# Performance work log

Measured on AMD Instinct MI355X. Metric: run time of the kernel, lower is better.

Reference implementation:

```python
import jax, jax.numpy as jnp
import numpy as np
from jax import lax

DN = ('NCHW', 'OIHW', 'NCHW')

def conv3x3(x, w):
    return lax.conv_general_dilated(x, w, (1, 1), 'SAME', dimension_numbers=DN)

def conv1x1(x, w, b):
    # w: [O, C], x: [B, C, H, W]
    return jnp.einsum('oc,bchw->bohw', w, x) + b[None, :, None, None]

def bn_relu(x, p):
    # p: [2, C] -> (scale, shift), eval-mode folded BatchNorm + ReLU
    return jax.nn.relu(x * p[0][None, :, None, None] + p[1][None, :, None, None])

def pam(y, Wb, bb, Wc, bc, Wd, bd, alpha):
    B, C, H, W = y.shape
    n = H * W
    b_ = conv1x1(y, Wb, bb).reshape(B, -1, n)   # [B, C/8, N]
    c_ = conv1x1(y, Wc, bc).reshape(B, -1, n)   # [B, C/8, N]
    d_ = conv1x1(y, Wd, bd).reshape(B, C, n)    # [B, C, N]
    energy = jnp.einsum('bkn,bkm->bnm', b_, c_)  # [B, N, N]
    attn = jax.nn.softmax(energy, axis=-1)
    feat = jnp.einsum('bcm,bnm->bcn', d_, attn).reshape(B, C, H, W)
    return alpha[0] * feat + y

def cam(y, beta):
    B, C, H, W = y.shape
    xf = y.reshape(B, C, H * W)
    energy = jnp.einsum('bcn,bdn->bcd', xf, xf)  # [B, C, C]
    energy = jnp.max(energy, axis=-1, keepdims=True) - energy
    attn = jax.nn.softmax(energy, axis=-1)
    feat = jnp.einsum('bcd,bdn->bcn', attn, xf).reshape(B, C, H, W)
    return beta[0] * feat + y

def reference(x, Wp1, bnp1, Wc1, bnc1, Wb, bb, Wc, bc, Wd, bd, alpha, beta,
              Wp2, bnp2, Wc2, bnc2, Wout, bout, Wp3, bp3, Wc3, bc3):
    feat_p = bn_relu(conv3x3(x, Wp1), bnp1)
    feat_p = pam(feat_p, Wb, bb, Wc, bc, Wd, bd, alpha)
    feat_p = bn_relu(conv3x3(feat_p, Wp2), bnp2)

    feat_c = bn_relu(conv3x3(x, Wc1), bnc1)
    feat_c = cam(feat_c, beta)
    feat_c = bn_relu(conv3x3(feat_c, Wc2), bnc2)

    fusion = feat_p + feat_c
    out_main = jax.nn.sigmoid(conv1x1(fusion, Wout, bout))
    out_p = jax.nn.sigmoid(conv1x1(feat_p, Wp3, bp3))
    out_c = jax.nn.sigmoid(conv1x1(feat_c, Wc3, bc3))
    return (out_main, out_p, out_c)

def setup_inputs() -> dict:
    key = jax.random.key(0)
    ks = jax.random.split(key, 24)
    Cin, Ci, Ck, NC = 512, 128, 16, 19
    B, H, W = 8, 64, 64
    s = lambda k, shape, scale=0.05: jax.random.normal(k, shape, jnp.float32) * scale
    return {
        'x': jax.random.normal(ks[0], (B, Cin, H, W), jnp.float32),
        'Wp1': s(ks[1], (Ci, Cin, 3, 3)), 'bnp1': jnp.stack([jnp.ones(Ci), jnp.zeros(Ci)]),
        'Wc1': s(ks[2], (Ci, Cin, 3, 3)), 'bnc1': jnp.stack([jnp.ones(Ci), jnp.zeros(Ci)]),
        'Wb': s(ks[3], (Ck, Ci)), 'bb': s(ks[4], (Ck,)),
        'Wc': s(ks[5], (Ck, Ci)), 'bc': s(ks[6], (Ck,)),
        'Wd': s(ks[7], (Ci, Ci)), 'bd': s(ks[8], (Ci,)),
        'alpha': jax.random.normal(ks[9], (1,), jnp.float32) * 0.5,
        'beta': jax.random.normal(ks[10], (1,), jnp.float32) * 0.5,
        'Wp2': s(ks[11], (Ci, Ci, 3, 3)), 'bnp2': jnp.stack([jnp.ones(Ci), jnp.zeros(Ci)]),
        'Wc2': s(ks[12], (Ci, Ci, 3, 3)), 'bnc2': jnp.stack([jnp.ones(Ci), jnp.zeros(Ci)]),
        'Wout': s(ks[13], (NC, Ci)), 'bout': s(ks[14], (NC,)),
        'Wp3': s(ks[15], (NC, Ci)), 'bp3': s(ks[16], (NC,)),
        'Wc3': s(ks[17], (NC, Ci)), 'bc3': s(ks[18], (NC,)),
    }
```

## Files before the change

kernel.cpp:

```cpp
#include <hip/hip_runtime.h>
#include <math.h>


typedef __attribute__((ext_vector_type(8)))  short short8;
typedef __attribute__((ext_vector_type(16))) float f32x16;

__device__ inline unsigned short f2bf(float f) {
    union { float f; unsigned u; } v; v.f = f;
    unsigned r = v.u + 0x7fffu + ((v.u >> 16) & 1u);
    return (unsigned short)(r >> 16);
}
__device__ inline float bf2f(unsigned short h) {
    union { unsigned u; float f; } v; v.u = ((unsigned)h) << 16;
    return v.f;
}

__global__ __launch_bounds__(256) void wpack_kernel(
    const float* __restrict__ W, unsigned short* __restrict__ wp, int Cin, int total)
{
    int idx = blockIdx.x * 256 + threadIdx.x;
    if (idx >= total) return;
    int chunk = idx / 18432;
    int rem   = idx - chunk * 18432;
    int tap   = rem >> 11;
    int rem2  = rem & 2047;
    int g     = rem2 >> 10;
    int co    = (rem2 >> 3) & 127;
    int ci8   = rem2 & 7;
    int cin   = (chunk << 4) + (g << 3) + ci8;
    wp[idx] = f2bf(W[((size_t)co * Cin + cin) * 9 + tap]);
}

__global__ __launch_bounds__(256) void wpack_split_kernel(
    const float* __restrict__ W, unsigned short* __restrict__ wph,
    unsigned short* __restrict__ wpl, int Cin, int total)
{
    int idx = blockIdx.x * 256 + threadIdx.x;
    if (idx >= total) return;
    int chunk = idx / 18432;
    int rem   = idx - chunk * 18432;
    int tap   = rem >> 11;
    int rem2  = rem & 2047;
    int g     = rem2 >> 10;
    int co    = (rem2 >> 3) & 127;
    int ci8   = rem2 & 7;
    int cin   = (chunk << 4) + (g << 3) + ci8;
    float w = W[((size_t)co * Cin + cin) * 9 + tap];
    unsigned short hi = f2bf(w);
    wph[idx] = hi;
    wpl[idx] = f2bf(w - bf2f(hi));
}

__global__ __launch_bounds__(256, 4) void conv3x3_merged(
    const float* __restrict__ xin,
    const unsigned short* __restrict__ wpp,
    const unsigned short* __restrict__ wph, const unsigned short* __restrict__ wpl,
    const float* __restrict__ bnp, const float* __restrict__ bnc,
    float* __restrict__ outP, float* __restrict__ outC,
    unsigned short* __restrict__ outh, unsigned short* __restrict__ outl)
{
    const int t   = threadIdx.x;
    const int w2  = t >> 6;
    const int xh  = w2 & 1;
    const int wy  = w2 >> 1;
    const int ln  = t & 63;
    const int l31 = ln & 31;
    const int g   = ln >> 5;
    const int y   = blockIdx.x;
    const int co0 = blockIdx.y << 6;
    const int b   = blockIdx.z;

    const int sr   = t >> 6;
    const int sx   = t & 63;
    const int sgy  = y - 1 + sr;
    const bool sv  = (t < 192) && ((unsigned)sgy < 64u);
    const int spid = sr * 66 + sx + 1;

    __shared__ __align__(16) unsigned short Xh[2][3168];
    __shared__ __align__(16) unsigned short Xo[2][3168];

    for (int i = t; i < 792; i += 256) {
        uint4 z; z.x = 0; z.y = 0; z.z = 0; z.w = 0;
        ((uint4*)Xh)[i] = z;
        ((uint4*)Xo)[i] = z;
    }

    const int co = co0 + (wy << 5) + l31;
    const unsigned short* wPb = wpp + (size_t)(g << 10) + ((size_t)co << 3);
    const unsigned short* wHb = wph + (size_t)(g << 10) + ((size_t)co << 3);
    const unsigned short* wLb = wpl + (size_t)(g << 10) + ((size_t)co << 3);
    const float* xsrc = xin + ((size_t)b << 21) + (sgy << 6) + sx;

    const f32x16 zero = {0,0,0,0,0,0,0,0,0,0,0,0,0,0,0,0};
    f32x16 ap = zero, ac = zero;

    float xv[16];
    if (sv) {
#pragma unroll
        for (int c = 0; c < 16; c++) xv[c] = xsrc[(size_t)c << 12];
    }
    __syncthreads();

    if (sv) {
        unsigned short th[16], tl[16];
#pragma unroll
        for (int c = 0; c < 16; c++) {
            unsigned short hi = f2bf(xv[c]);
            th[c] = hi; tl[c] = f2bf(xv[c] - bf2f(hi));
        }
        *(uint4*)&Xh[0][spid << 3]          = ((uint4*)th)[0];
        *(uint4*)&Xh[0][1584 + (spid << 3)] = ((uint4*)th)[1];
        *(uint4*)&Xo[0][spid << 3]          = ((uint4*)tl)[0];
        *(uint4*)&Xo[0][1584 + (spid << 3)] = ((uint4*)tl)[1];
    }

    int cur = 0;
    for (int ch = 0; ch < 32; ++ch) {
        __syncthreads();
        const bool pf = (ch < 31);
        if (pf && sv) {
#pragma unroll
            for (int c = 0; c < 16; c++)
                xv[c] = xsrc[((size_t)(ch + 1) << 16) + ((size_t)c << 12)];
        }
        const size_t wo = (size_t)ch * 18432;
#pragma unroll 3
        for (int tap = 0; tap < 9; ++tap) {
            const int dy = tap / 3, dx = tap - dy * 3;
            const int xi = (g ? 1584 : 0) + (((dy * 66) + (xh << 5) + l31 + dx) << 3);
            short8 vap = *(const short8*)(wPb + wo + tap * 2048);
            short8 vah = *(const short8*)(wHb + wo + tap * 2048);
            short8 val = *(const short8*)(wLb + wo + tap * 2048);
            short8 bh_ = *(const short8*)&Xh[cur][xi];
            short8 bl_ = *(const short8*)&Xo[cur][xi];
            ap = __builtin_amdgcn_mfma_f32_32x32x16_bf16(vap, bh_, ap, 0, 0, 0);
            ac = __builtin_amdgcn_mfma_f32_32x32x16_bf16(vah, bh_, ac, 0, 0, 0);
            ac = __builtin_amdgcn_mfma_f32_32x32x16_bf16(vah, bl_, ac, 0, 0, 0);
            ac = __builtin_amdgcn_mfma_f32_32x32x16_bf16(val, bh_, ac, 0, 0, 0);
        }
        if (pf && sv) {
            unsigned short th[16], tl[16];
#pragma unroll
            for (int c = 0; c < 16; c++) {
                unsigned short hi = f2bf(xv[c]);
                th[c] = hi; tl[c] = f2bf(xv[c] - bf2f(hi));
            }
            const int nb = cur ^ 1;
            *(uint4*)&Xh[nb][spid << 3]          = ((uint4*)th)[0];
            *(uint4*)&Xh[nb][1584 + (spid << 3)] = ((uint4*)th)[1];
            *(uint4*)&Xo[nb][spid << 3]          = ((uint4*)tl)[0];
            *(uint4*)&Xo[nb][1584 + (spid << 3)] = ((uint4*)tl)[1];
        }
        cur ^= 1;
    }

    const int x = (xh << 5) + l31;
#pragma unroll
    for (int r = 0; r < 16; r++) {
        int c2 = co0 + (wy << 5) + (r & 3) + ((r >> 2) << 3) + (g << 2);
        size_t o = (((size_t)b * 128 + c2) << 12) + (y << 6) + x;
        float vp = fmaf(ap[r], bnp[c2], bnp[128 + c2]);
        vp = vp > 0.f ? vp : 0.f;
        outP[o] = vp;
        float vc = fmaf(ac[r], bnc[c2], bnc[128 + c2]);
        vc = vc > 0.f ? vc : 0.f;
        outC[o] = vc;
        unsigned short hi = f2bf(vc);
        outh[o] = hi;
        outl[o] = f2bf(vc - bf2f(hi));
    }
}

__global__ __launch_bounds__(256, 4) void conv3x3_bf(
    const unsigned short* __restrict__ xin, int Cin,
    const unsigned short* __restrict__ wpk, const float* __restrict__ bn,
    float* __restrict__ out_f32)
{
    const int t   = threadIdx.x;
    const int w2  = t >> 6;
    const int xh  = w2 & 1;
    const int wy  = w2 >> 1;
    const int ln  = t & 63;
    const int l31 = ln & 31;
    const int g   = ln >> 5;
    const int y   = blockIdx.x;
    const int co0 = blockIdx.y << 6;
    const int b   = blockIdx.z;

    const int sr   = t >> 6;
    const int sx   = t & 63;
    const int sgy  = y - 1 + sr;
    const bool sv  = (t < 192) && ((unsigned)sgy < 64u);
    const int spid = sr * 66 + sx + 1;

    __shared__ __align__(16) unsigned short Xl[2][3168];

    for (int i = t; i < 792; i += 256) {
        uint4 z; z.x = 0; z.y = 0; z.z = 0; z.w = 0;
        ((uint4*)Xl)[i] = z;
    }

    const int co = co0 + (wy << 5) + l31;
    const unsigned short* wB = wpk + (size_t)(g << 10) + ((size_t)co << 3);
    const unsigned short* xsrc = xin + (((size_t)b * Cin) << 12) + (sgy << 6) + sx;

    const f32x16 zero = {0,0,0,0,0,0,0,0,0,0,0,0,0,0,0,0};
    f32x16 acc = zero;

    unsigned short xv[16];
    if (sv) {
#pragma unroll
        for (int c = 0; c < 16; c++) xv[c] = xsrc[(size_t)c << 12];
    }
    __syncthreads();

    if (sv) {
        *(uint4*)&Xl[0][spid << 3]          = ((uint4*)xv)[0];
        *(uint4*)&Xl[0][1584 + (spid << 3)] = ((uint4*)xv)[1];
    }

    const int nchunks = Cin >> 4;
    int cur = 0;
    for (int ch = 0; ch < nchunks; ++ch) {
        __syncthreads();
        const bool pf = (ch < nchunks - 1);
        if (pf && sv) {
#pragma unroll
            for (int c = 0; c < 16; c++)
                xv[c] = xsrc[((size_t)(ch + 1) << 16) + ((size_t)c << 12)];
        }
        const size_t wo = (size_t)ch * 18432;
#pragma unroll 3
        for (int tap = 0; tap < 9; ++tap) {
            const int dy = tap / 3, dx = tap - dy * 3;
            const int xi = (g ? 1584 : 0) + (((dy * 66) + (xh << 5) + l31 + dx) << 3);
            short8 a  = *(const short8*)(wB + wo + tap * 2048);
            short8 b0 = *(const short8*)&Xl[cur][xi];
            acc = __builtin_amdgcn_mfma_f32_32x32x16_bf16(a, b0, acc, 0, 0, 0);
        }
        if (pf && sv) {
            const int nb = cur ^ 1;
            *(uint4*)&Xl[nb][spid << 3]          = ((uint4*)xv)[0];
            *(uint4*)&Xl[nb][1584 + (spid << 3)] = ((uint4*)xv)[1];
        }
        cur ^= 1;
    }

    const int x = (xh << 5) + l31;
#pragma unroll
    for (int r = 0; r < 16; r++) {
        int c2 = co0 + (wy << 5) + (r & 3) + ((r >> 2) << 3) + (g << 2);
        float v = fmaf(acc[r], bn[c2], bn[128 + c2]);
        v = v > 0.f ? v : 0.f;
        out_f32[(((size_t)b * 128 + c2) << 12) + (y << 6) + x] = v;
    }
}

__global__ __launch_bounds__(256, 4) void conv3x3_hilo_bf(
    const unsigned short* __restrict__ xhg, const unsigned short* __restrict__ xlg,
    int Cin, const unsigned short* __restrict__ wph, const unsigned short* __restrict__ wpl,
    const float* __restrict__ bn, float* __restrict__ out_f32)
{
    const int t   = threadIdx.x;
    const int w2  = t >> 6;
    const int xh  = w2 & 1;
    const int wy  = w2 >> 1;
    const int ln  = t & 63;
    const int l31 = ln & 31;
    const int g   = ln >> 5;
    const int y   = blockIdx.x;
    const int co0 = blockIdx.y << 6;
    const int b   = blockIdx.z;

    const int sr   = t >> 6;
    const int sx   = t & 63;
    const int sgy  = y - 1 + sr;
    const bool sv  = (t < 192) && ((unsigned)sgy < 64u);
    const int spid = sr * 66 + sx + 1;

    __shared__ __align__(16) unsigned short Xa[2][3168];
    __shared__ __align__(16) unsigned short Xb[2][3168];

    for (int i = t; i < 792; i += 256) {
        uint4 z; z.x = 0; z.y = 0; z.z = 0; z.w = 0;
        ((uint4*)Xa)[i] = z;
        ((uint4*)Xb)[i] = z;
    }

    const int co = co0 + (wy << 5) + l31;
    const unsigned short* wHb = wph + (size_t)(g << 10) + ((size_t)co << 3);
    const unsigned short* wLb = wpl + (size_t)(g << 10) + ((size_t)co << 3);
    const unsigned short* hsrc = xhg + (((size_t)b * Cin) << 12) + (sgy << 6) + sx;
    const unsigned short* lsrc = xlg + (((size_t)b * Cin) << 12) + (sgy << 6) + sx;

    const f32x16 zero = {0,0,0,0,0,0,0,0,0,0,0,0,0,0,0,0};
    f32x16 acc = zero;

    unsigned short hv[16], lv[16];
    if (sv) {
#pragma unroll
        for (int c = 0; c < 16; c++) { hv[c] = hsrc[(size_t)c << 12]; lv[c] = lsrc[(size_t)c << 12]; }
    }
    __syncthreads();

    if (sv) {
        *(uint4*)&Xa[0][spid << 3]          = ((uint4*)hv)[0];
        *(uint4*)&Xa[0][1584 + (spid << 3)] = ((uint4*)hv)[1];
        *(uint4*)&Xb[0][spid << 3]          = ((uint4*)lv)[0];
        *(uint4*)&Xb[0][1584 + (spid << 3)] = ((uint4*)lv)[1];
    }

    const int nchunks = Cin >> 4;
    int cur = 0;
    for (int ch = 0; ch < nchunks; ++ch) {
        __syncthreads();
        const bool pf = (ch < nchunks - 1);
        if (pf && sv) {
#pragma unroll
            for (int c = 0; c < 16; c++) {
                hv[c] = hsrc[((size_t)(ch + 1) << 16) + ((size_t)c << 12)];
                lv[c] = lsrc[((size_t)(ch + 1) << 16) + ((size_t)c << 12)];
            }
        }
        const size_t wo = (size_t)ch * 18432;
#pragma unroll 3
        for (int tap = 0; tap < 9; ++tap) {
            const int dy = tap / 3, dx = tap - dy * 3;
            const int xi = (g ? 1584 : 0) + (((dy * 66) + (xh << 5) + l31 + dx) << 3);
            short8 ah  = *(const short8*)(wHb + wo + tap * 2048);
            short8 al  = *(const short8*)(wLb + wo + tap * 2048);
            short8 bh_ = *(const short8*)&Xa[cur][xi];
            short8 bl_ = *(const short8*)&Xb[cur][xi];
            acc = __builtin_amdgcn_mfma_f32_32x32x16_bf16(ah, bh_, acc, 0, 0, 0);
            acc = __builtin_amdgcn_mfma_f32_32x32x16_bf16(ah, bl_, acc, 0, 0, 0);
            acc = __builtin_amdgcn_mfma_f32_32x32x16_bf16(al, bh_, acc, 0, 0, 0);
        }
        if (pf && sv) {
            const int nb = cur ^ 1;
            *(uint4*)&Xa[nb][spid << 3]          = ((uint4*)hv)[0];
            *(uint4*)&Xa[nb][1584 + (spid << 3)] = ((uint4*)hv)[1];
            *(uint4*)&Xb[nb][spid << 3]          = ((uint4*)lv)[0];
            *(uint4*)&Xb[nb][1584 + (spid << 3)] = ((uint4*)lv)[1];
        }
        cur ^= 1;
    }

    const int x = (xh << 5) + l31;
#pragma unroll
    for (int r = 0; r < 16; r++) {
        int c2 = co0 + (wy << 5) + (r & 3) + ((r >> 2) << 3) + (g << 2);
        float v = fmaf(acc[r], bn[c2], bn[128 + c2]);
        v = v > 0.f ? v : 0.f;
        out_f32[(((size_t)b * 128 + c2) << 12) + (y << 6) + x] = v;
    }
}

__global__ __launch_bounds__(256) void cam_energy_mfma(
    const unsigned short* __restrict__ bh, const unsigned short* __restrict__ bl,
    float* __restrict__ egy_part)
{
    const int t   = threadIdx.x;
    const int w   = t >> 6;
    const int ln  = t & 63;
    const int l31 = ln & 31;
    const int g   = ln >> 5;
    const int bx  = blockIdx.x;
    int i0c, j0c;
    if (bx < 4)      { i0c = 0; j0c = bx; }
    else if (bx < 7) { i0c = 1; j0c = bx - 3; }
    else if (bx < 9) { i0c = 2; j0c = bx - 5; }
    else             { i0c = 3; j0c = 3; }
    const int i0  = i0c << 5;
    const int j0  = j0c << 5;
    const int nseg = blockIdx.y;
    const int b   = blockIdx.z;

    __shared__ float red[4][64][17];

    const f32x16 zero = {0,0,0,0,0,0,0,0,0,0,0,0,0,0,0,0};
    f32x16 acc = zero;
    const int nb = (nseg << 9) + (w << 7) + (g << 3);
    const size_t ri = ((size_t)b * 128 + i0 + l31) << 12;
    const size_t rj = ((size_t)b * 128 + j0 + l31) << 12;

#pragma unroll
    for (int c = 0; c < 8; c++) {
        const int n0 = nb + (c << 4);
        short8 ah  = *(const short8*)(bh + ri + n0);
        short8 al  = *(const short8*)(bl + ri + n0);
        short8 bhf = *(const short8*)(bh + rj + n0);
        short8 blf = *(const short8*)(bl + rj + n0);
        acc = __builtin_amdgcn_mfma_f32_32x32x16_bf16(ah, bhf, acc, 0, 0, 0);
        acc = __builtin_amdgcn_mfma_f32_32x32x16_bf16(ah, blf, acc, 0, 0, 0);
        acc = __builtin_amdgcn_mfma_f32_32x32x16_bf16(al, bhf, acc, 0, 0, 0);
    }
#pragma unroll
    for (int r = 0; r < 16; r++) red[w][ln][r] = acc[r];
    __syncthreads();

    const int lane = t & 63;
    const int rq   = t >> 6;
    float* base = egy_part + (((size_t)(nseg * 8 + b)) << 14);
#pragma unroll
    for (int e = 0; e < 4; e++) {
        const int reg = (rq << 2) + e;
        float v = red[0][lane][reg] + red[1][lane][reg]
                + red[2][lane][reg] + red[3][lane][reg];
        const int i = i0 + (reg & 3) + ((reg >> 2) << 3) + ((lane >> 5) << 2);
        const int j = j0 + (lane & 31);
        base[i * 128 + j] = v;
        if (i0c != j0c) base[j * 128 + i] = v;
    }
}

__global__ __launch_bounds__(256) void cam_softmax_fused(
    const float* __restrict__ egy_part, float* __restrict__ egy)
{
    const int b   = blockIdx.x;
    const int rg  = blockIdx.y;
    const int t   = threadIdx.x;
    const int row = (rg << 4) + (t >> 4);
    const int jg  = t & 15;

    float e[8];
#pragma unroll
    for (int jj = 0; jj < 8; jj++) e[jj] = 0.f;
    for (int seg = 0; seg < 8; seg++) {
        const float* p = egy_part + (((size_t)(seg * 8 + b)) << 14) + row * 128 + (jg << 3);
#pragma unroll
        for (int jj = 0; jj < 8; jj++) e[jj] += p[jj];
    }
    float mn = e[0];
#pragma unroll
    for (int jj = 1; jj < 8; jj++) mn = fminf(mn, e[jj]);
#pragma unroll
    for (int k = 1; k < 16; k <<= 1) mn = fminf(mn, __shfl_xor(mn, k));
    float s = 0.f;
#pragma unroll
    for (int jj = 0; jj < 8; jj++) { float p = __expf(mn - e[jj]); e[jj] = p; s += p; }
#pragma unroll
    for (int k = 1; k < 16; k <<= 1) s += __shfl_xor(s, k);
    const float inv = 1.f / s;
    float* orow = egy + ((size_t)b << 14) + row * 128 + (jg << 3);
#pragma unroll
    for (int jj = 0; jj < 8; jj++) orow[jj] = e[jj] * inv;
}

__global__ __launch_bounds__(256) void pam_qk_1x1(
    const float* __restrict__ A, const float* __restrict__ Wb, const float* __restrict__ bb,
    const float* __restrict__ Wc, const float* __restrict__ bc,
    unsigned short* __restrict__ qt, unsigned short* __restrict__ kt)
{
    __shared__ float wl[2 * 16 * 128];
    __shared__ float bl[32];
    const int t = threadIdx.x;
    const int n = (blockIdx.x << 8) + t;
    const int b = blockIdx.y;
    for (int idx = t; idx < 2048; idx += 256) { wl[idx] = Wb[idx]; wl[2048 + idx] = Wc[idx]; }
    if (t < 16) { bl[t] = bb[t]; bl[16 + t] = bc[t]; }
    __syncthreads();
    float ab[16], ac[16];
#pragma unroll
    for (int k = 0; k < 16; k++) { ab[k] = 0.f; ac[k] = 0.f; }
    for (int chn = 0; chn < 128; ++chn) {
        float a = A[(((size_t)b * 128 + chn) << 12) + n];
#pragma unroll
        for (int k = 0; k < 16; k++) {
            ab[k] = fmaf(wl[k * 128 + chn], a, ab[k]);
            ac[k] = fmaf(wl[2048 + k * 128 + chn], a, ac[k]);
        }
    }
    unsigned short uq[16], uk[16];
#pragma unroll
    for (int k = 0; k < 16; k++) {
        uq[k] = f2bf(ab[k] + bl[k]);
        uk[k] = f2bf(ac[k] + bl[16 + k]);
    }
    size_t row = (size_t)b * 4096 + n;
    ((uint4*)qt)[row * 2 + 0] = ((uint4*)uq)[0];
    ((uint4*)qt)[row * 2 + 1] = ((uint4*)uq)[1];
    ((uint4*)kt)[row * 2 + 0] = ((uint4*)uk)[0];
    ((uint4*)kt)[row * 2 + 1] = ((uint4*)uk)[1];
}

__global__ __launch_bounds__(256) void pam_v_1x1(
    const float* __restrict__ A, const float* __restrict__ Wd, const float* __restrict__ bd,
    unsigned short* __restrict__ vb)
{
    __shared__ float wl[32 * 128];
    __shared__ float bl[32];
    const int t   = threadIdx.x;
    const int n   = (blockIdx.x << 8) + t;
    const int co0 = blockIdx.y << 5;
    const int b   = blockIdx.z;
    for (int idx = t; idx < 4096; idx += 256) {
        int c2 = idx >> 7, chv = idx & 127;
        wl[idx] = Wd[(co0 + c2) * 128 + chv];
    }
    if (t < 32) bl[t] = bd[co0 + t];
    __syncthreads();
    float acc[32];
#pragma unroll
    for (int k = 0; k < 32; k++) acc[k] = 0.f;
    for (int chn = 0; chn < 128; ++chn) {
        float a = A[(((size_t)b * 128 + chn) << 12) + n];
#pragma unroll
        for (int k = 0; k < 32; k++) acc[k] = fmaf(wl[k * 128 + chn], a, acc[k]);
    }
#pragma unroll
    for (int k = 0; k < 32; k++)
        vb[(((size_t)b * 128 + co0 + k) << 12) + n] = f2bf(acc[k] + bl[k]);
}

__global__ __launch_bounds__(256) void pam_attn_mfma(
    const unsigned short* __restrict__ qt, const unsigned short* __restrict__ kt,
    const unsigned short* __restrict__ vb,
    const float* __restrict__ alpha, const float* __restrict__ Y,
    unsigned short* __restrict__ outb)
{
    const int t  = threadIdx.x;
    const int w  = t >> 6;
    const int L  = t & 63;
    const int ln = L & 31;
    const int g  = L >> 5;
    const int b  = blockIdx.y;
    const int n0 = blockIdx.x << 6;
    const int c0 = w << 5;

    __shared__ unsigned short Pf[2][16 * 512];
    __shared__ float red[2][4][64];
    __shared__ float redS[4][64];

    const f32x16 zero = {0,0,0,0,0,0,0,0,0,0,0,0,0,0,0,0};
    short8 q0 = *(const short8*)(qt + (((size_t)b * 4096 + n0 + ln) << 4) + (g << 3));
    short8 q1 = *(const short8*)(qt + (((size_t)b * 4096 + n0 + 32 + ln) << 4) + (g << 3));
    const float al = alpha[0];

    f32x16 acc0 = zero, acc1 = zero;
    float rs0 = 0.f, rs1 = 0.f;
    float mold0 = -3.0e38f, mold1 = -3.0e38f;

    int par = 0;
    for (int m0 = 0; m0 < 4096; m0 += 128) {
        const int mq = m0 + (w << 5);
        short8 kfrag = *(const short8*)(kt + (((size_t)b * 4096 + mq + ln) << 4) + (g << 3));
        f32x16 s0 = __builtin_amdgcn_mfma_f32_32x32x16_bf16(kfrag, q0, zero, 0, 0, 0);
        f32x16 s1 = __builtin_amdgcn_mfma_f32_32x32x16_bf16(kfrag, q1, zero, 0, 0, 0);

        float lm0 = s0[0], lm1 = s1[0];
#pragma unroll
        for (int r = 1; r < 16; r++) { lm0 = fmaxf(lm0, s0[r]); lm1 = fmaxf(lm1, s1[r]); }
        lm0 = fmaxf(lm0, __shfl_xor(lm0, 32));
        lm1 = fmaxf(lm1, __shfl_xor(lm1, 32));
        if (L < 32) { red[par][w][L] = lm0; red[par][w][32 + L] = lm1; }
        __syncthreads();
        const float mb0 = fmaxf(fmaxf(red[par][0][ln], red[par][1][ln]),
                                fmaxf(red[par][2][ln], red[par][3][ln]));
        const float mb1 = fmaxf(fmaxf(red[par][0][32 + ln], red[par][1][32 + ln]),
                                fmaxf(red[par][2][32 + ln], red[par][3][32 + ln]));
        const float mnew0 = fmaxf(mold0, mb0);
        const float mnew1 = fmaxf(mold1, mb1);
        const float fs0 = __expf(mold0 - mnew0);
        const float fs1 = __expf(mold1 - mnew1);
        mold0 = mnew0; mold1 = mnew1;
        rs0 *= fs0; rs1 *= fs1;
#pragma unroll
        for (int r = 0; r < 16; r++) { acc0[r] *= fs0; acc1[r] *= fs1; }

        {
            float p[16];
#pragma unroll
            for (int r = 0; r < 16; r++) { p[r] = __expf(s0[r] - mnew0); rs0 += p[r]; }
            float xx[16];
#pragma unroll
            for (int r = 0; r < 16; r++) xx[r] = __shfl_xor(p[r], 32);
            unsigned short f0[8], f1[8];
#pragma unroll
            for (int i = 0; i < 4; i++) {
                f0[i]     = f2bf(g ? xx[4 + i]  : p[i]);
                f0[4 + i] = f2bf(g ? p[4 + i]   : xx[i]);
                f1[i]     = f2bf(g ? xx[12 + i] : p[8 + i]);
                f1[4 + i] = f2bf(g ? p[12 + i]  : xx[8 + i]);
            }
            *(short8*)(&Pf[par][((w << 2) + g) * 512 + (ln << 3)])     = *(short8*)f0;
            *(short8*)(&Pf[par][((w << 2) + 2 + g) * 512 + (ln << 3)]) = *(short8*)f1;
        }
        {
            float p[16];
#pragma unroll
            for (int r = 0; r < 16; r++) { p[r] = __expf(s1[r] - mnew1); rs1 += p[r]; }
            float xx[16];
#pragma unroll
            for (int r = 0; r < 16; r++) xx[r] = __shfl_xor(p[r], 32);
            unsigned short f0[8], f1[8];
#pragma unroll
            for (int i = 0; i < 4; i++) {
                f0[i]     = f2bf(g ? xx[4 + i]  : p[i]);
                f0[4 + i] = f2bf(g ? p[4 + i]   : xx[i]);
                f1[i]     = f2bf(g ? xx[12 + i] : p[8 + i]);
                f1[4 + i] = f2bf(g ? p[12 + i]  : xx[8 + i]);
            }
            *(short8*)(&Pf[par][((w << 2) + g) * 512 + 256 + (ln << 3)])     = *(short8*)f0;
            *(short8*)(&Pf[par][((w << 2) + 2 + g) * 512 + 256 + (ln << 3)]) = *(short8*)f1;
        }
        __syncthreads();

#pragma unroll
        for (int kk = 0; kk < 8; kk++) {
            short8 vfrag = *(const short8*)(vb + (((size_t)b * 128 + c0 + ln) << 12)
                                               + m0 + (kk << 4) + (g << 3));
            short8 pf0 = *(const short8*)(&Pf[par][((kk << 1) + g) * 512 + (ln << 3)]);
            short8 pf1 = *(const short8*)(&Pf[par][((kk << 1) + g) * 512 + 256 + (ln << 3)]);
            acc0 = __builtin_amdgcn_mfma_f32_32x32x16_bf16(vfrag, pf0, acc0, 0, 0, 0);
            acc1 = __builtin_amdgcn_mfma_f32_32x32x16_bf16(vfrag, pf1, acc1, 0, 0, 0);
        }
        par ^= 1;
    }

    rs0 += __shfl_xor(rs0, 32);
    rs1 += __shfl_xor(rs1, 32);
    if (L < 32) { redS[w][L] = rs0; redS[w][32 + L] = rs1; }
    __syncthreads();
    const float inv0 = 1.f / (redS[0][ln] + redS[1][ln] + redS[2][ln] + redS[3][ln]);
    const float inv1 = 1.f / (redS[0][32 + ln] + redS[1][32 + ln]
                            + redS[2][32 + ln] + redS[3][32 + ln]);
#pragma unroll
    for (int r = 0; r < 16; r++) {
        int c = c0 + (r & 3) + ((r >> 2) << 3) + (g << 2);
        size_t idx0 = (((size_t)b * 128 + c) << 12) + n0 + ln;
        outb[idx0]      = f2bf(fmaf(al, acc0[r] * inv0, Y[idx0]));
        outb[idx0 + 32] = f2bf(fmaf(al, acc1[r] * inv1, Y[idx0 + 32]));
    }
}

__global__ __launch_bounds__(256) void cam_feat(
    const float* __restrict__ attn, const float* __restrict__ Bf,
    const float* __restrict__ beta, unsigned short* __restrict__ oh,
    unsigned short* __restrict__ ol)
{
    const int t  = threadIdx.x;
    const int n  = (blockIdx.x << 8) + t;
    const int c0 = blockIdx.y << 5;
    const int b  = blockIdx.z;
    __shared__ float al[32 * 128];
    for (int idx = t; idx < 4096; idx += 256)
        al[idx] = attn[(size_t)b * 16384 + (c0 + (idx >> 7)) * 128 + (idx & 127)];
    __syncthreads();
    float acc[32];
#pragma unroll
    for (int k = 0; k < 32; k++) acc[k] = 0.f;
    for (int d = 0; d < 128; ++d) {
        float v = Bf[(((size_t)b * 128 + d) << 12) + n];
#pragma unroll
        for (int k = 0; k < 32; k++) acc[k] = fmaf(al[k * 128 + d], v, acc[k]);
    }
    float be = beta[0];
#pragma unroll
    for (int k = 0; k < 32; k++) {
        size_t idx = (((size_t)b * 128 + c0 + k) << 12) + n;
        float v = fmaf(be, acc[k], Bf[idx]);
        unsigned short hi = f2bf(v);
        oh[idx] = hi;
        ol[idx] = f2bf(v - bf2f(hi));
    }
}

__global__ __launch_bounds__(256) void heads(
    const float* __restrict__ FP, const float* __restrict__ FC,
    const float* __restrict__ Wout, const float* __restrict__ bout,
    const float* __restrict__ Wp3, const float* __restrict__ bp3,
    const float* __restrict__ Wc3, const float* __restrict__ bc3,
    float* __restrict__ out)
{
    const int t = threadIdx.x;
    const int n = (blockIdx.x << 8) + t;
    const int b = blockIdx.y;
    __shared__ float wl[3 * 19 * 128];
    __shared__ float bl[3 * 19];
    for (int idx = t; idx < 2432; idx += 256) {
        wl[idx]        = Wout[idx];
        wl[2432 + idx] = Wp3[idx];
        wl[4864 + idx] = Wc3[idx];
    }
    if (t < 19) { bl[t] = bout[t]; bl[19 + t] = bp3[t]; bl[38 + t] = bc3[t]; }
    __syncthreads();
    float am[19], ap[19], ac[19];
#pragma unroll
    for (int o = 0; o < 19; o++) { am[o] = 0.f; ap[o] = 0.f; ac[o] = 0.f; }
    for (int chn = 0; chn < 128; ++chn) {
        float pv = FP[(((size_t)b * 128 + chn) << 12) + n];
        float cv = FC[(((size_t)b * 128 + chn) << 12) + n];
        float fv = pv + cv;
#pragma unroll
        for (int o = 0; o < 19; o++) {
            am[o] = fmaf(wl[o * 128 + chn], fv, am[o]);
            ap[o] = fmaf(wl[2432 + o * 128 + chn], pv, ap[o]);
            ac[o] = fmaf(wl[4864 + o * 128 + chn], cv, ac[o]);
        }
    }
    const size_t OS = (size_t)8 * 19 * 4096;
#pragma unroll
    for (int o = 0; o < 19; o++) {
        size_t base = (((size_t)b * 19 + o) << 12) + n;
        out[base]          = 1.f / (1.f + __expf(-(am[o] + bl[o])));
        out[OS + base]     = 1.f / (1.f + __expf(-(ap[o] + bl[19 + o])));
        out[2 * OS + base] = 1.f / (1.f + __expf(-(ac[o] + bl[38 + o])));
    }
}

extern "C" void kernel_launch(void* const* d_in, const int* in_sizes, int n_in,
                              void* d_out, int out_size, void* d_ws, size_t ws_size,
                              hipStream_t stream)
{
    const float* x     = (const float*)d_in[0];
    const float* Wp1   = (const float*)d_in[1];
    const float* bnp1  = (const float*)d_in[2];
    const float* Wc1   = (const float*)d_in[3];
    const float* bnc1  = (const float*)d_in[4];
    const float* Wb    = (const float*)d_in[5];
    const float* bb    = (const float*)d_in[6];
    const float* Wc    = (const float*)d_in[7];
    const float* bcv   = (const float*)d_in[8];
    const float* Wd    = (const float*)d_in[9];
    const float* bd    = (const float*)d_in[10];
    const float* alpha = (const float*)d_in[11];
    const float* beta  = (const float*)d_in[12];
    const float* Wp2   = (const float*)d_in[13];
    const float* bnp2  = (const float*)d_in[14];
    const float* Wc2   = (const float*)d_in[15];
    const float* bnc2  = (const float*)d_in[16];
    const float* Wout  = (const float*)d_in[17];
    const float* bo    = (const float*)d_in[18];
    const float* Wp3   = (const float*)d_in[19];
    const float* bp3   = (const float*)d_in[20];
    const float* Wc3   = (const float*)d_in[21];
    const float* bc3   = (const float*)d_in[22];
    float* out = (float*)d_out;

    char* ws = (char*)d_ws;
    const size_t MB = 1u << 20;
    const size_t W1SZ = (size_t)32 * 18432 * 2;
    const size_t W2SZ = (size_t)8 * 18432 * 2;
    float*          bufA     = (float*)(ws);
    float*          bufB     = (float*)(ws + 16 * MB);
    unsigned short* vb       = (unsigned short*)(ws + 32 * MB);
    float*          egy_part = (float*)(ws + 40 * MB);
    float*          bufD     = (float*)(ws + 32 * MB);
    unsigned short* bh       = (unsigned short*)(ws + 48 * MB);
    unsigned short* blo      = (unsigned short*)(ws + 56 * MB);
    unsigned short* pam_bf   = (unsigned short*)(ws + 48 * MB);
    unsigned short* c2h      = (unsigned short*)(ws + 48 * MB);
    unsigned short* c2l      = (unsigned short*)(ws + 56 * MB);
    unsigned short* qt       = (unsigned short*)(ws + 64 * MB);
    unsigned short* kt       = (unsigned short*)(ws + 65 * MB);
    float*          egy      = (float*)(ws + 66 * MB + (1u << 17));
    unsigned short* wp1      = (unsigned short*)(ws + 67 * MB);
    unsigned short* wc1h     = (unsigned short*)(ws + 67 * MB + W1SZ);
    unsigned short* wc1l     = (unsigned short*)(ws + 67 * MB + 2 * W1SZ);
    unsigned short* wp2      = (unsigned short*)(ws + 67 * MB + 3 * W1SZ);
    unsigned short* wc2h     = (unsigned short*)(ws + 67 * MB + 3 * W1SZ + W2SZ);
    unsigned short* wc2l     = (unsigned short*)(ws + 67 * MB + 3 * W1SZ + 2 * W2SZ);

    dim3 blk(256);
    const int n1 = 32 * 18432;
    const int n2 = 8 * 18432;
    wpack_kernel<<<dim3((n1 + 255) / 256), blk, 0, stream>>>(Wp1, wp1, 512, n1);
    wpack_kernel<<<dim3((n2 + 255) / 256), blk, 0, stream>>>(Wp2, wp2, 128, n2);
    wpack_split_kernel<<<dim3((n1 + 255) / 256), blk, 0, stream>>>(Wc1, wc1h, wc1l, 512, n1);
    wpack_split_kernel<<<dim3((n2 + 255) / 256), blk, 0, stream>>>(Wc2, wc2h, wc2l, 128, n2);

    conv3x3_merged<<<dim3(64, 2, 8), blk, 0, stream>>>(x, wp1, wc1h, wc1l, bnp1, bnc1,
                                                       bufA, bufB, bh, blo);
    cam_energy_mfma<<<dim3(10, 8, 8), blk, 0, stream>>>(bh, blo, egy_part);
    cam_softmax_fused<<<dim3(8, 8), blk, 0, stream>>>(egy_part, egy);
    pam_qk_1x1<<<dim3(16, 8), blk, 0, stream>>>(bufA, Wb, bb, Wc, bcv, qt, kt);
    pam_v_1x1<<<dim3(16, 4, 8), blk, 0, stream>>>(bufA, Wd, bd, vb);
    pam_attn_mfma<<<dim3(64, 8), blk, 0, stream>>>(qt, kt, vb, alpha, bufA, pam_bf);
    conv3x3_bf<<<dim3(64, 2, 8), blk, 0, stream>>>(pam_bf, 128, wp2, bnp2, bufD);
    cam_feat<<<dim3(16, 4, 8), blk, 0, stream>>>(egy, bufB, beta, c2h, c2l);
    conv3x3_hilo_bf<<<dim3(64, 2, 8), blk, 0, stream>>>(c2h, c2l, 128, wc2h, wc2l, bnc2, bufA);
    heads<<<dim3(16, 8), blk, 0, stream>>>(bufD, bufA, Wout, bo, Wp3, bp3, Wc3, bc3, out);
}
```

Before: 730.5 us.

## Stage conv3x3 weight chunks in LDS via direct global-to-LDS loads

```diff
diff --git a/kernel.cpp b/kernel.cpp
--- a/kernel.cpp
+++ b/kernel.cpp
@@ -4,6 +4,10 @@
 
 typedef __attribute__((ext_vector_type(8)))  short short8;
 typedef __attribute__((ext_vector_type(16))) float f32x16;
+
+#define GLD_LDS16(gp, lp) __builtin_amdgcn_global_load_lds( \
+    (const __attribute__((address_space(1))) void*)(gp),    \
+    (__attribute__((address_space(3))) void*)(lp), 16, 0, 0)
 
 __device__ inline unsigned short f2bf(float f) {
     union { float f; unsigned u; } v; v.f = f;
@@ -51,7 +55,7 @@
     wpl[idx] = f2bf(w - bf2f(hi));
 }
 
-__global__ __launch_bounds__(256, 4) void conv3x3_merged(
+__global__ __launch_bounds__(256, 2) void conv3x3_merged(
     const float* __restrict__ xin,
     const unsigned short* __restrict__ wpp,
     const unsigned short* __restrict__ wph, const unsigned short* __restrict__ wpl,
@@ -78,6 +82,7 @@
 
     __shared__ __align__(16) unsigned short Xh[2][3168];
     __shared__ __align__(16) unsigned short Xo[2][3168];
+    __shared__ __align__(16) unsigned short WL[27648];
 
     for (int i = t; i < 792; i += 256) {
         uint4 z; z.x = 0; z.y = 0; z.z = 0; z.w = 0;
@@ -85,11 +90,11 @@
         ((uint4*)Xo)[i] = z;
     }
 
-    const int co = co0 + (wy << 5) + l31;
-    const unsigned short* wPb = wpp + (size_t)(g << 10) + ((size_t)co << 3);
-    const unsigned short* wHb = wph + (size_t)(g << 10) + ((size_t)co << 3);
-    const unsigned short* wLb = wpl + (size_t)(g << 10) + ((size_t)co << 3);
     const float* xsrc = xin + ((size_t)b << 21) + (sgy << 6) + sx;
+    const int co8  = (((wy << 5) + l31) << 3);
+    const int lnw  = ln << 3;
+
+    const int cbase = co0 << 3;
 
     const f32x16 zero = {0,0,0,0,0,0,0,0,0,0,0,0,0,0,0,0};
     f32x16 ap = zero, ac = zero;
@@ -98,6 +103,13 @@
     if (sv) {
 #pragma unroll
         for (int c = 0; c < 16; c++) xv[c] = xsrc[(size_t)c << 12];
+    }
+    for (int s = w2; s < 54; s += 4) {
+        const int arr = s / 18;
+        const int sub = s - arr * 18;
+        const unsigned short* src = (arr == 0) ? wpp : ((arr == 1) ? wph : wpl);
+        GLD_LDS16(src + sub * 1024 + cbase + lnw,
+                  (uint4*)(WL + arr * 9216 + sub * 512));
     }
     __syncthreads();
 
@@ -123,20 +135,31 @@
             for (int c = 0; c < 16; c++)
                 xv[c] = xsrc[((size_t)(ch + 1) << 16) + ((size_t)c << 12)];
         }
-        const size_t wo = (size_t)ch * 18432;
 #pragma unroll 3
         for (int tap = 0; tap < 9; ++tap) {
             const int dy = tap / 3, dx = tap - dy * 3;
             const int xi = (g ? 1584 : 0) + (((dy * 66) + (xh << 5) + l31 + dx) << 3);
-            short8 vap = *(const short8*)(wPb + wo + tap * 2048);
-            short8 vah = *(const short8*)(wHb + wo + tap * 2048);
-            short8 val = *(const short8*)(wLb + wo + tap * 2048);
+            const int wb = ((tap << 1) + g) * 512 + co8;
+            short8 vap = *(const short8*)&WL[wb];
+            short8 vah = *(const short8*)&WL[9216 + wb];
+            short8 val = *(const short8*)&WL[18432 + wb];
             short8 bh_ = *(const short8*)&Xh[cur][xi];
             short8 bl_ = *(const short8*)&Xo[cur][xi];
             ap = __builtin_amdgcn_mfma_f32_32x32x16_bf16(vap, bh_, ap, 0, 0, 0);
             ac = __builtin_amdgcn_mfma_f32_32x32x16_bf16(vah, bh_, ac, 0, 0, 0);
             ac = __builtin_amdgcn_mfma_f32_32x32x16_bf16(vah, bl_, ac, 0, 0, 0);
             ac = __builtin_amdgcn_mfma_f32_32x32x16_bf16(val, bh_, ac, 0, 0, 0);
+        }
+        __syncthreads();
+        if (pf) {
+            const size_t wo = (size_t)(ch + 1) * 18432;
+            for (int s = w2; s < 54; s += 4) {
+                const int arr = s / 18;
+                const int sub = s - arr * 18;
+                const unsigned short* src = (arr == 0) ? wpp : ((arr == 1) ? wph : wpl);
+                GLD_LDS16(src + wo + sub * 1024 + cbase + lnw,
+                          (uint4*)(WL + arr * 9216 + sub * 512));
+            }
         }
         if (pf && sv) {
             unsigned short th[16], tl[16];
@@ -171,7 +194,7 @@
     }
 }
 
-__global__ __launch_bounds__(256, 4) void conv3x3_bf(
+__global__ __launch_bounds__(256, 5) void conv3x3_bf(
     const unsigned short* __restrict__ xin, int Cin,
     const unsigned short* __restrict__ wpk, const float* __restrict__ bn,
     float* __restrict__ out_f32)
@@ -194,15 +217,17 @@
     const int spid = sr * 66 + sx + 1;
 
     __shared__ __align__(16) unsigned short Xl[2][3168];
+    __shared__ __align__(16) unsigned short WL[9216];
 
     for (int i = t; i < 792; i += 256) {
         uint4 z; z.x = 0; z.y = 0; z.z = 0; z.w = 0;
         ((uint4*)Xl)[i] = z;
     }
 
-    const int co = co0 + (wy << 5) + l31;
-    const unsigned short* wB = wpk + (size_t)(g << 10) + ((size_t)co << 3);
     const unsigned short* xsrc = xin + (((size_t)b * Cin) << 12) + (sgy << 6) + sx;
+    const int co8  = (((wy << 5) + l31) << 3);
+    const int lnw  = ln << 3;
+    const int cbase = co0 << 3;
 
     const f32x16 zero = {0,0,0,0,0,0,0,0,0,0,0,0,0,0,0,0};
     f32x16 acc = zero;
@@ -212,6 +237,8 @@
 #pragma unroll
         for (int c = 0; c < 16; c++) xv[c] = xsrc[(size_t)c << 12];
     }
+    for (int s = w2; s < 18; s += 4)
+        GLD_LDS16(wpk + s * 1024 + cbase + lnw, (uint4*)(WL + s * 512));
     __syncthreads();
 
     if (sv) {
@@ -229,14 +256,19 @@
             for (int c = 0; c < 16; c++)
                 xv[c] = xsrc[((size_t)(ch + 1) << 16) + ((size_t)c << 12)];
         }
-        const size_t wo = (size_t)ch * 18432;
 #pragma unroll 3
         for (int tap = 0; tap < 9; ++tap) {
             const int dy = tap / 3, dx = tap - dy * 3;
             const int xi = (g ? 1584 : 0) + (((dy * 66) + (xh << 5) + l31 + dx) << 3);
-            short8 a  = *(const short8*)(wB + wo + tap * 2048);
+            short8 a  = *(const short8*)&WL[((tap << 1) + g) * 512 + co8];
             short8 b0 = *(const short8*)&Xl[cur][xi];
             acc = __builtin_amdgcn_mfma_f32_32x32x16_bf16(a, b0, acc, 0, 0, 0);
+        }
+        __syncthreads();
+        if (pf) {
+            const size_t wo = (size_t)(ch + 1) * 18432;
+            for (int s = w2; s < 18; s += 4)
+                GLD_LDS16(wpk + wo + s * 1024 + cbase + lnw, (uint4*)(WL + s * 512));
         }
         if (pf && sv) {
             const int nb = cur ^ 1;
@@ -256,7 +288,7 @@
     }
 }
 
-__global__ __launch_bounds__(256, 4) void conv3x3_hilo_bf(
+__global__ __launch_bounds__(256, 2) void conv3x3_hilo_bf(
     const unsigned short* __restrict__ xhg, const unsigned short* __restrict__ xlg,
     int Cin, const unsigned short* __restrict__ wph, const unsigned short* __restrict__ wpl,
     const float* __restrict__ bn, float* __restrict__ out_f32)
@@ -280,6 +312,7 @@
 
     __shared__ __align__(16) unsigned short Xa[2][3168];
     __shared__ __align__(16) unsigned short Xb[2][3168];
+    __shared__ __align__(16) unsigned short WL[18432];
 
     for (int i = t; i < 792; i += 256) {
         uint4 z; z.x = 0; z.y = 0; z.z = 0; z.w = 0;
@@ -287,11 +320,11 @@
         ((uint4*)Xb)[i] = z;
     }
 
-    const int co = co0 + (wy << 5) + l31;
-    const unsigned short* wHb = wph + (size_t)(g << 10) + ((size_t)co << 3);
-    const unsigned short* wLb = wpl + (size_t)(g << 10) + ((size_t)co << 3);
     const unsigned short* hsrc = xhg + (((size_t)b * Cin) << 12) + (sgy << 6) + sx;
     const unsigned short* lsrc = xlg + (((size_t)b * Cin) << 12) + (sgy << 6) + sx;
+    const int co8  = (((wy << 5) + l31) << 3);
+    const int lnw  = ln << 3;
+    const int cbase = co0 << 3;
 
     const f32x16 zero = {0,0,0,0,0,0,0,0,0,0,0,0,0,0,0,0};
     f32x16 acc = zero;
@@ -300,6 +333,12 @@
     if (sv) {
 #pragma unroll
         for (int c = 0; c < 16; c++) { hv[c] = hsrc[(size_t)c << 12]; lv[c] = lsrc[(size_t)c << 12]; }
+    }
+    for (int s = w2; s < 36; s += 4) {
+        const int arr = s / 18;
+        const int sub = s - arr * 18;
+        const unsigned short* src = arr ? wpl : wph;
+        GLD_LDS16(src + sub * 1024 + cbase + lnw, (uint4*)(WL + arr * 9216 + sub * 512));
     }
     __syncthreads();
 
@@ -322,18 +361,29 @@
                 lv[c] = lsrc[((size_t)(ch + 1) << 16) + ((size_t)c << 12)];
             }
         }
-        const size_t wo = (size_t)ch * 18432;
 #pragma unroll 3
         for (int tap = 0; tap < 9; ++tap) {
             const int dy = tap / 3, dx = tap - dy * 3;
             const int xi = (g ? 1584 : 0) + (((dy * 66) + (xh << 5) + l31 + dx) << 3);
-            short8 ah  = *(const short8*)(wHb + wo + tap * 2048);
-            short8 al  = *(const short8*)(wLb + wo + tap * 2048);
+            const int wb = ((tap << 1) + g) * 512 + co8;
+            short8 ah  = *(const short8*)&WL[wb];
+            short8 al  = *(const short8*)&WL[9216 + wb];
             short8 bh_ = *(const short8*)&Xa[cur][xi];
             short8 bl_ = *(const short8*)&Xb[cur][xi];
             acc = __builtin_amdgcn_mfma_f32_32x32x16_bf16(ah, bh_, acc, 0, 0, 0);
             acc = __builtin_amdgcn_mfma_f32_32x32x16_bf16(ah, bl_, acc, 0, 0, 0);
             acc = __builtin_amdgcn_mfma_f32_32x32x16_bf16(al, bh_, acc, 0, 0, 0);
+        }
+        __syncthreads();
+        if (pf) {
+            const size_t wo = (size_t)(ch + 1) * 18432;
+            for (int s = w2; s < 36; s += 4) {
+                const int arr = s / 18;
+                const int sub = s - arr * 18;
+                const unsigned short* src = arr ? wpl : wph;
+                GLD_LDS16(src + wo + sub * 1024 + cbase + lnw,
+                          (uint4*)(WL + arr * 9216 + sub * 512));
+            }
         }
         if (pf && sv) {
             const int nb = cur ^ 1;
```

Result: slower. 761.3 us (+4.2%).

## Cover all 128 output channels per conv block with two x-halves per wave

Applied to the files above, without the earlier changes.

```diff
diff --git a/kernel.cpp b/kernel.cpp
--- a/kernel.cpp
+++ b/kernel.cpp
@@ -51,7 +51,7 @@
     wpl[idx] = f2bf(w - bf2f(hi));
 }
 
-__global__ __launch_bounds__(256, 4) void conv3x3_merged(
+__global__ __launch_bounds__(256, 2) void conv3x3_merged(
     const float* __restrict__ xin,
     const unsigned short* __restrict__ wpp,
     const unsigned short* __restrict__ wph, const unsigned short* __restrict__ wpl,
@@ -61,13 +61,10 @@
 {
     const int t   = threadIdx.x;
     const int w2  = t >> 6;
-    const int xh  = w2 & 1;
-    const int wy  = w2 >> 1;
     const int ln  = t & 63;
     const int l31 = ln & 31;
     const int g   = ln >> 5;
     const int y   = blockIdx.x;
-    const int co0 = blockIdx.y << 6;
     const int b   = blockIdx.z;
 
     const int sr   = t >> 6;
@@ -85,14 +82,14 @@
         ((uint4*)Xo)[i] = z;
     }
 
-    const int co = co0 + (wy << 5) + l31;
+    const int co = (w2 << 5) + l31;
     const unsigned short* wPb = wpp + (size_t)(g << 10) + ((size_t)co << 3);
     const unsigned short* wHb = wph + (size_t)(g << 10) + ((size_t)co << 3);
     const unsigned short* wLb = wpl + (size_t)(g << 10) + ((size_t)co << 3);
     const float* xsrc = xin + ((size_t)b << 21) + (sgy << 6) + sx;
 
     const f32x16 zero = {0,0,0,0,0,0,0,0,0,0,0,0,0,0,0,0};
-    f32x16 ap = zero, ac = zero;
+    f32x16 ap0 = zero, ap1 = zero, ac0 = zero, ac1 = zero;
 
     float xv[16];
     if (sv) {
@@ -127,16 +124,23 @@
 #pragma unroll 3
         for (int tap = 0; tap < 9; ++tap) {
             const int dy = tap / 3, dx = tap - dy * 3;
-            const int xi = (g ? 1584 : 0) + (((dy * 66) + (xh << 5) + l31 + dx) << 3);
+            const int xi0 = (g ? 1584 : 0) + (((dy * 66) + l31 + dx) << 3);
+            const int xi1 = xi0 + 256;
             short8 vap = *(const short8*)(wPb + wo + tap * 2048);
             short8 vah = *(const short8*)(wHb + wo + tap * 2048);
             short8 val = *(const short8*)(wLb + wo + tap * 2048);
-            short8 bh_ = *(const short8*)&Xh[cur][xi];
-            short8 bl_ = *(const short8*)&Xo[cur][xi];
-            ap = __builtin_amdgcn_mfma_f32_32x32x16_bf16(vap, bh_, ap, 0, 0, 0);
-            ac = __builtin_amdgcn_mfma_f32_32x32x16_bf16(vah, bh_, ac, 0, 0, 0);
-            ac = __builtin_amdgcn_mfma_f32_32x32x16_bf16(vah, bl_, ac, 0, 0, 0);
-            ac = __builtin_amdgcn_mfma_f32_32x32x16_bf16(val, bh_, ac, 0, 0, 0);
+            short8 b0h = *(const short8*)&Xh[cur][xi0];
+            short8 b1h = *(const short8*)&Xh[cur][xi1];
+            short8 b0l = *(const short8*)&Xo[cur][xi0];
+            short8 b1l = *(const short8*)&Xo[cur][xi1];
+            ap0 = __builtin_amdgcn_mfma_f32_32x32x16_bf16(vap, b0h, ap0, 0, 0, 0);
+            ap1 = __builtin_amdgcn_mfma_f32_32x32x16_bf16(vap, b1h, ap1, 0, 0, 0);
+            ac0 = __builtin_amdgcn_mfma_f32_32x32x16_bf16(vah, b0h, ac0, 0, 0, 0);
+            ac1 = __builtin_amdgcn_mfma_f32_32x32x16_bf16(vah, b1h, ac1, 0, 0, 0);
+            ac0 = __builtin_amdgcn_mfma_f32_32x32x16_bf16(vah, b0l, ac0, 0, 0, 0);
+            ac1 = __builtin_amdgcn_mfma_f32_32x32x16_bf16(vah, b1l, ac1, 0, 0, 0);
+            ac0 = __builtin_amdgcn_mfma_f32_32x32x16_bf16(val, b0h, ac0, 0, 0, 0);
+            ac1 = __builtin_amdgcn_mfma_f32_32x32x16_bf16(val, b1h, ac1, 0, 0, 0);
         }
         if (pf && sv) {
             unsigned short th[16], tl[16];
@@ -154,37 +158,39 @@
         cur ^= 1;
     }
 
-    const int x = (xh << 5) + l31;
-#pragma unroll
-    for (int r = 0; r < 16; r++) {
-        int c2 = co0 + (wy << 5) + (r & 3) + ((r >> 2) << 3) + (g << 2);
-        size_t o = (((size_t)b * 128 + c2) << 12) + (y << 6) + x;
-        float vp = fmaf(ap[r], bnp[c2], bnp[128 + c2]);
-        vp = vp > 0.f ? vp : 0.f;
-        outP[o] = vp;
-        float vc = fmaf(ac[r], bnc[c2], bnc[128 + c2]);
-        vc = vc > 0.f ? vc : 0.f;
-        outC[o] = vc;
-        unsigned short hi = f2bf(vc);
-        outh[o] = hi;
-        outl[o] = f2bf(vc - bf2f(hi));
-    }
-}
-
-__global__ __launch_bounds__(256, 4) void conv3x3_bf(
+#pragma unroll
+    for (int j = 0; j < 2; j++) {
+        const f32x16 aP = j ? ap1 : ap0;
+        const f32x16 aC = j ? ac1 : ac0;
+        const int x = (j << 5) + l31;
+#pragma unroll
+        for (int r = 0; r < 16; r++) {
+            int c2 = (w2 << 5) + (r & 3) + ((r >> 2) << 3) + (g << 2);
+            size_t o = (((size_t)b * 128 + c2) << 12) + (y << 6) + x;
+            float vp = fmaf(aP[r], bnp[c2], bnp[128 + c2]);
+            vp = vp > 0.f ? vp : 0.f;
+            outP[o] = vp;
+            float vc = fmaf(aC[r], bnc[c2], bnc[128 + c2]);
+            vc = vc > 0.f ? vc : 0.f;
+            outC[o] = vc;
+            unsigned short hi = f2bf(vc);
+            outh[o] = hi;
+            outl[o] = f2bf(vc - bf2f(hi));
+        }
+    }
+}
+
+__global__ __launch_bounds__(256, 2) void conv3x3_bf(
     const unsigned short* __restrict__ xin, int Cin,
     const unsigned short* __restrict__ wpk, const float* __restrict__ bn,
     float* __restrict__ out_f32)
 {
     const int t   = threadIdx.x;
     const int w2  = t >> 6;
-    const int xh  = w2 & 1;
-    const int wy  = w2 >> 1;
     const int ln  = t & 63;
     const int l31 = ln & 31;
     const int g   = ln >> 5;
     const int y   = blockIdx.x;
-    const int co0 = blockIdx.y << 6;
     const int b   = blockIdx.z;
 
     const int sr   = t >> 6;
@@ -200,12 +206,12 @@
         ((uint4*)Xl)[i] = z;
     }
 
-    const int co = co0 + (wy << 5) + l31;
+    const int co = (w2 << 5) + l31;
     const unsigned short* wB = wpk + (size_t)(g << 10) + ((size_t)co << 3);
     const unsigned short* xsrc = xin + (((size_t)b * Cin) << 12) + (sgy << 6) + sx;
 
     const f32x16 zero = {0,0,0,0,0,0,0,0,0,0,0,0,0,0,0,0};
-    f32x16 acc = zero;
+    f32x16 acc0 = zero, acc1 = zero;
 
     unsigned short xv[16];
     if (sv) {
@@ -233,10 +239,12 @@
 #pragma unroll 3
         for (int tap = 0; tap < 9; ++tap) {
             const int dy = tap / 3, dx = tap - dy * 3;
-            const int xi = (g ? 1584 : 0) + (((dy * 66) + (xh << 5) + l31 + dx) << 3);
+            const int xi0 = (g ? 1584 : 0) + (((dy * 66) + l31 + dx) << 3);
             short8 a  = *(const short8*)(wB + wo + tap * 2048);
-            short8 b0 = *(const short8*)&Xl[cur][xi];
-            acc = __builtin_amdgcn_mfma_f32_32x32x16_bf16(a, b0, acc, 0, 0, 0);
+            short8 b0 = *(const short8*)&Xl[cur][xi0];
+            short8 b1 = *(const short8*)&Xl[cur][xi0 + 256];
+            acc0 = __builtin_amdgcn_mfma_f32_32x32x16_bf16(a, b0, acc0, 0, 0, 0);
+            acc1 = __builtin_amdgcn_mfma_f32_32x32x16_bf16(a, b1, acc1, 0, 0, 0);
         }
         if (pf && sv) {
             const int nb = cur ^ 1;
@@ -246,30 +254,31 @@
         cur ^= 1;
     }
 
-    const int x = (xh << 5) + l31;
-#pragma unroll
-    for (int r = 0; r < 16; r++) {
-        int c2 = co0 + (wy << 5) + (r & 3) + ((r >> 2) << 3) + (g << 2);
-        float v = fmaf(acc[r], bn[c2], bn[128 + c2]);
-        v = v > 0.f ? v : 0.f;
-        out_f32[(((size_t)b * 128 + c2) << 12) + (y << 6) + x] = v;
-    }
-}
-
-__global__ __launch_bounds__(256, 4) void conv3x3_hilo_bf(
+#pragma unroll
+    for (int j = 0; j < 2; j++) {
+        const f32x16 a = j ? acc1 : acc0;
+        const int x = (j << 5) + l31;
+#pragma unroll
+        for (int r = 0; r < 16; r++) {
+            int c2 = (w2 << 5) + (r & 3) + ((r >> 2) << 3) + (g << 2);
+            float v = fmaf(a[r], bn[c2], bn[128 + c2]);
+            v = v > 0.f ? v : 0.f;
+            out_f32[(((size_t)b * 128 + c2) << 12) + (y << 6) + x] = v;
+        }
+    }
+}
+
+__global__ __launch_bounds__(256, 2) void conv3x3_hilo_bf(
     const unsigned short* __restrict__ xhg, const unsigned short* __restrict__ xlg,
     int Cin, const unsigned short* __restrict__ wph, const unsigned short* __restrict__ wpl,
     const float* __restrict__ bn, float* __restrict__ out_f32)
 {
     const int t   = threadIdx.x;
     const int w2  = t >> 6;
-    const int xh  = w2 & 1;
-    const int wy  = w2 >> 1;
     const int ln  = t & 63;
     const int l31 = ln & 31;
     const int g   = ln >> 5;
     const int y   = blockIdx.x;
-    const int co0 = blockIdx.y << 6;
     const int b   = blockIdx.z;
 
     const int sr   = t >> 6;
@@ -287,14 +296,14 @@
         ((uint4*)Xb)[i] = z;
     }
 
-    const int co = co0 + (wy << 5) + l31;
+    const int co = (w2 << 5) + l31;
     const unsigned short* wHb = wph + (size_t)(g << 10) + ((size_t)co << 3);
     const unsigned short* wLb = wpl + (size_t)(g << 10) + ((size_t)co << 3);
     const unsigned short* hsrc = xhg + (((size_t)b * Cin) << 12) + (sgy << 6) + sx;
     const unsigned short* lsrc = xlg + (((size_t)b * Cin) << 12) + (sgy << 6) + sx;
 
     const f32x16 zero = {0,0,0,0,0,0,0,0,0,0,0,0,0,0,0,0};
-    f32x16 acc = zero;
+    f32x16 acc0 = zero, acc1 = zero;
 
     unsigned short hv[16], lv[16];
     if (sv) {
@@ -326,14 +335,20 @@
 #pragma unroll 3
         for (int tap = 0; tap < 9; ++tap) {
             const int dy = tap / 3, dx = tap - dy * 3;
-            const int xi = (g ? 1584 : 0) + (((dy * 66) + (xh << 5) + l31 + dx) << 3);
+            const int xi0 = (g ? 1584 : 0) + (((dy * 66) + l31 + dx) << 3);
+            const int xi1 = xi0 + 256;
             short8 ah  = *(const short8*)(wHb + wo + tap * 2048);
             short8 al  = *(const short8*)(wLb + wo + tap * 2048);
-            short8 bh_ = *(const short8*)&Xa[cur][xi];
-            short8 bl_ = *(const short8*)&Xb[cur][xi];
-            acc = __builtin_amdgcn_mfma_f32_32x32x16_bf16(ah, bh_, acc, 0, 0, 0);
-            acc = __builtin_amdgcn_mfma_f32_32x32x16_bf16(ah, bl_, acc, 0, 0, 0);
-            acc = __builtin_amdgcn_mfma_f32_32x32x16_bf16(al, bh_, acc, 0, 0, 0);
+            short8 b0h = *(const short8*)&Xa[cur][xi0];
+            short8 b1h = *(const short8*)&Xa[cur][xi1];
+            short8 b0l = *(const short8*)&Xb[cur][xi0];
+            short8 b1l = *(const short8*)&Xb[cur][xi1];
+            acc0 = __builtin_amdgcn_mfma_f32_32x32x16_bf16(ah, b0h, acc0, 0, 0, 0);
+            acc1 = __builtin_amdgcn_mfma_f32_32x32x16_bf16(ah, b1h, acc1, 0, 0, 0);
+            acc0 = __builtin_amdgcn_mfma_f32_32x32x16_bf16(ah, b0l, acc0, 0, 0, 0);
+            acc1 = __builtin_amdgcn_mfma_f32_32x32x16_bf16(ah, b1l, acc1, 0, 0, 0);
+            acc0 = __builtin_amdgcn_mfma_f32_32x32x16_bf16(al, b0h, acc0, 0, 0, 0);
+            acc1 = __builtin_amdgcn_mfma_f32_32x32x16_bf16(al, b1h, acc1, 0, 0, 0);
         }
         if (pf && sv) {
             const int nb = cur ^ 1;
@@ -345,13 +360,17 @@
         cur ^= 1;
     }
 
-    const int x = (xh << 5) + l31;
-#pragma unroll
-    for (int r = 0; r < 16; r++) {
-        int c2 = co0 + (wy << 5) + (r & 3) + ((r >> 2) << 3) + (g << 2);
-        float v = fmaf(acc[r], bn[c2], bn[128 + c2]);
-        v = v > 0.f ? v : 0.f;
-        out_f32[(((size_t)b * 128 + c2) << 12) + (y << 6) + x] = v;
+#pragma unroll
+    for (int j = 0; j < 2; j++) {
+        const f32x16 a = j ? acc1 : acc0;
+        const int x = (j << 5) + l31;
+#pragma unroll
+        for (int r = 0; r < 16; r++) {
+            int c2 = (w2 << 5) + (r & 3) + ((r >> 2) << 3) + (g << 2);
+            float v = fmaf(a[r], bn[c2], bn[128 + c2]);
+            v = v > 0.f ? v : 0.f;
+            out_f32[(((size_t)b * 128 + c2) << 12) + (y << 6) + x] = v;
+        }
     }
 }
 
@@ -769,15 +788,15 @@
     wpack_split_kernel<<<dim3((n1 + 255) / 256), blk, 0, stream>>>(Wc1, wc1h, wc1l, 512, n1);
     wpack_split_kernel<<<dim3((n2 + 255) / 256), blk, 0, stream>>>(Wc2, wc2h, wc2l, 128, n2);
 
-    conv3x3_merged<<<dim3(64, 2, 8), blk, 0, stream>>>(x, wp1, wc1h, wc1l, bnp1, bnc1,
+    conv3x3_merged<<<dim3(64, 1, 8), blk, 0, stream>>>(x, wp1, wc1h, wc1l, bnp1, bnc1,
                                                        bufA, bufB, bh, blo);
     cam_energy_mfma<<<dim3(10, 8, 8), blk, 0, stream>>>(bh, blo, egy_part);
     cam_softmax_fused<<<dim3(8, 8), blk, 0, stream>>>(egy_part, egy);
     pam_qk_1x1<<<dim3(16, 8), blk, 0, stream>>>(bufA, Wb, bb, Wc, bcv, qt, kt);
     pam_v_1x1<<<dim3(16, 4, 8), blk, 0, stream>>>(bufA, Wd, bd, vb);
     pam_attn_mfma<<<dim3(64, 8), blk, 0, stream>>>(qt, kt, vb, alpha, bufA, pam_bf);
-    conv3x3_bf<<<dim3(64, 2, 8), blk, 0, stream>>>(pam_bf, 128, wp2, bnp2, bufD);
+    conv3x3_bf<<<dim3(64, 1, 8), blk, 0, stream>>>(pam_bf, 128, wp2, bnp2, bufD);
     cam_feat<<<dim3(16, 4, 8), blk, 0, stream>>>(egy, bufB, beta, c2h, c2l);
-    conv3x3_hilo_bf<<<dim3(64, 2, 8), blk, 0, stream>>>(c2h, c2l, 128, wc2h, wc2l, bnc2, bufA);
+    conv3x3_hilo_bf<<<dim3(64, 1, 8), blk, 0, stream>>>(c2h, c2l, 128, wc2h, wc2l, bnc2, bufA);
     heads<<<dim3(16, 8), blk, 0, stream>>>(bufD, bufA, Wout, bo, Wp3, bp3, Wc3, bc3, out);
 }
```

Result: slower. 748.2 us (+2.4%).
